# Kernel optimization log

Hardware: AMD Instinct MI355X
Metric: run time of the kernel (lower is better)

Reference implementation:

```python
import jax, jax.numpy as jnp
import numpy as np


def setup_inputs() -> dict:
    key = jax.random.key(0)
    k1, k2 = jax.random.split(key)
    bs, dim = 8192, 768
    nl_vec = jax.random.normal(k1, (bs, dim), dtype=jnp.float32)
    code_vec = jax.random.normal(k2, (bs, dim), dtype=jnp.float32)
    return {"nl_vec": nl_vec, "code_vec": code_vec}


def reference(nl_vec, code_vec):
    # scores[i, j] = <nl_vec[i], code_vec[j]>  (GEMM form of the broadcast mult-sum)
    scores = jnp.einsum("id,jd->ij", nl_vec, code_vec)  # [bs, bs]
    bs = scores.shape[0]
    # CrossEntropyLoss with labels = arange(bs): mean over rows of (logsumexp - diag)
    lse = jax.nn.logsumexp(scores, axis=-1)             # [bs]
    diag = jnp.einsum("id,id->i", nl_vec, code_vec)     # scores[i, i]
    loss = jnp.mean(lse - diag)
    return (loss, code_vec, nl_vec)
```

## Files before the change

### kernel.cpp

```cpp
#include <hip/hip_runtime.h>

#define BS     8192
#define DIM    768
#define NPART  16
#define BM     128
#define BN     128
#define BK     64
#define PCOLS  (BS / NPART)
#define NJT    (PCOLS / BN)
#define NKT    (DIM / BK)
#define L1B    128
#define L1R    (BS / L1B)

typedef __bf16 bfrag_t __attribute__((ext_vector_type(8)));
typedef float  facc_t  __attribute__((ext_vector_type(4)));

typedef const __attribute__((address_space(1))) void gv_t;
typedef __attribute__((address_space(3))) void lv_t;

__device__ __forceinline__ void gll16(const void* g, void* l) {
  __builtin_amdgcn_global_load_lds((gv_t*)g, (lv_t*)l, 16, 0, 0);
}

__device__ __forceinline__ unsigned short f2bf(float f) {
  union { float f; unsigned u; } v; v.f = f;
  unsigned u = v.u;
  return (unsigned short)((u + 0x7FFFu + ((u >> 16) & 1u)) >> 16);
}

__global__ void prep_kernel(const float* __restrict__ nl, const float* __restrict__ cd,
                            float* __restrict__ cd_copy, float* __restrict__ nl_copy,
                            unsigned short* __restrict__ nlb, unsigned short* __restrict__ cdb,
                            float* __restrict__ dg) {
  const int lane = threadIdx.x & 63;
  const int wave = threadIdx.x >> 6;
  const int row  = blockIdx.x * 4 + wave;
  const size_t rbase = (size_t)row * DIM;
  const float4* ar = reinterpret_cast<const float4*>(nl + rbase);
  const float4* br = reinterpret_cast<const float4*>(cd + rbase);
  float4* wa = reinterpret_cast<float4*>(nl_copy + rbase);
  float4* wb = reinterpret_cast<float4*>(cd_copy + rbase);
  ushort4* ba = reinterpret_cast<ushort4*>(nlb + rbase);
  ushort4* bb = reinterpret_cast<ushort4*>(cdb + rbase);

  float s = 0.f;
#pragma unroll
  for (int i = 0; i < 3; ++i) {
    int idx = lane + 64 * i;
    float4 x = ar[idx];
    float4 y = br[idx];
    wa[idx] = x;
    wb[idx] = y;
    ushort4 xb, yb;
    xb.x = f2bf(x.x); xb.y = f2bf(x.y); xb.z = f2bf(x.z); xb.w = f2bf(x.w);
    yb.x = f2bf(y.x); yb.y = f2bf(y.y); yb.z = f2bf(y.z); yb.w = f2bf(y.w);
    ba[idx] = xb;
    bb[idx] = yb;
    s += x.x * y.x + x.y * y.y + x.z * y.z + x.w * y.w;
  }
#pragma unroll
  for (int off = 32; off; off >>= 1) s += __shfl_xor(s, off, 64);
  if (lane == 0) dg[row] = s;
}

__global__ __launch_bounds__(256, 4) void gemm_lse_kernel(
    const unsigned short* __restrict__ Abf,
    const unsigned short* __restrict__ Bbf,
    float* __restrict__ pm, float* __restrict__ pl) {
  __shared__ __align__(16) unsigned short As[BM * BK];
  __shared__ __align__(16) unsigned short Bs[BN * BK];

  const int tid  = threadIdx.x;
  const int lane = tid & 63;
  const int wave = tid >> 6;
  const int wm   = wave >> 1;
  const int wn   = wave & 1;
  const int l15  = lane & 15;
  const int l4   = lane >> 4;
  const int sw   = l15 & 7;
  const int cp   = blockIdx.x;
  const int rb   = blockIdx.y;

  int srow[4], sc8g[4];
#pragma unroll
  for (int t = 0; t < 4; ++t) {
    int u   = wave * 256 + t * 64 + lane;
    srow[t] = u >> 3;
    sc8g[t] = (u & 7) ^ (srow[t] & 7);
  }

  float mrun[4][4], lrun[4][4];
#pragma unroll
  for (int i = 0; i < 4; ++i)
#pragma unroll
    for (int r = 0; r < 4; ++r) { mrun[i][r] = -1e30f; lrun[i][r] = 0.f; }

  for (int jt = 0; jt < NJT; ++jt) {
    facc_t acc[4][4];
#pragma unroll
    for (int mt = 0; mt < 4; ++mt)
#pragma unroll
      for (int nt = 0; nt < 4; ++nt) acc[mt][nt] = (facc_t){0.f, 0.f, 0.f, 0.f};

    for (int kt = 0; kt < NKT; ++kt) {
      __syncthreads();
#pragma unroll
      for (int t = 0; t < 4; ++t) {
        size_t ldso = (size_t)(wave * 256 + t * 64) * 8;
        gll16(Abf + (size_t)(rb * BM + srow[t]) * DIM + kt * BK + sc8g[t] * 8, As + ldso);
        gll16(Bbf + (size_t)(cp * PCOLS + jt * BN + srow[t]) * DIM + kt * BK + sc8g[t] * 8, Bs + ldso);
      }
      __syncthreads();

#pragma unroll
      for (int ks = 0; ks < 2; ++ks) {
        const int k8 = ks * 4 + l4;
        bfrag_t af[4], bfv[4];
#pragma unroll
        for (int mt = 0; mt < 4; ++mt) {
          int row = wm * 64 + mt * 16 + l15;
          af[mt] = *reinterpret_cast<const bfrag_t*>(&As[row * BK + (k8 ^ sw) * 8]);
        }
#pragma unroll
        for (int nt = 0; nt < 4; ++nt) {
          int row = wn * 64 + nt * 16 + l15;
          bfv[nt] = *reinterpret_cast<const bfrag_t*>(&Bs[row * BK + (k8 ^ sw) * 8]);
        }
#pragma unroll
        for (int mt = 0; mt < 4; ++mt)
#pragma unroll
          for (int nt = 0; nt < 4; ++nt)
            acc[mt][nt] = __builtin_amdgcn_mfma_f32_16x16x32_bf16(af[mt], bfv[nt], acc[mt][nt], 0, 0, 0);
      }
    }

#pragma unroll
    for (int mt = 0; mt < 4; ++mt)
#pragma unroll
      for (int r = 0; r < 4; ++r) {
        float v0 = acc[mt][0][r], v1 = acc[mt][1][r], v2 = acc[mt][2][r], v3 = acc[mt][3][r];
        float tm = fmaxf(fmaxf(v0, v1), fmaxf(v2, v3));
        float mn = fmaxf(mrun[mt][r], tm);
        float sc = __expf(mrun[mt][r] - mn);
        lrun[mt][r] = lrun[mt][r] * sc +
                      __expf(v0 - mn) + __expf(v1 - mn) + __expf(v2 - mn) + __expf(v3 - mn);
        mrun[mt][r] = mn;
      }
  }

#pragma unroll
  for (int mask = 1; mask < 16; mask <<= 1)
#pragma unroll
    for (int mt = 0; mt < 4; ++mt)
#pragma unroll
      for (int r = 0; r < 4; ++r) {
        float om = __shfl_xor(mrun[mt][r], mask, 64);
        float ol = __shfl_xor(lrun[mt][r], mask, 64);
        float mn = fmaxf(mrun[mt][r], om);
        lrun[mt][r] = lrun[mt][r] * __expf(mrun[mt][r] - mn) + ol * __expf(om - mn);
        mrun[mt][r] = mn;
      }

  float* cm = reinterpret_cast<float*>(As);
  float* cl = reinterpret_cast<float*>(Bs);
  __syncthreads();
  if (l15 == 0) {
#pragma unroll
    for (int mt = 0; mt < 4; ++mt)
#pragma unroll
      for (int r = 0; r < 4; ++r) {
        int rl = wm * 64 + mt * 16 + l4 * 4 + r;
        cm[wn * BM + rl] = mrun[mt][r];
        cl[wn * BM + rl] = lrun[mt][r];
      }
  }
  __syncthreads();
  if (tid < BM) {
    float m0 = cm[tid], l0 = cl[tid];
    float m1 = cm[BM + tid], l1 = cl[BM + tid];
    float mn = fmaxf(m0, m1);
    float ll = l0 * __expf(m0 - mn) + l1 * __expf(m1 - mn);
    size_t g = (size_t)(rb * BM + tid) * NPART + cp;
    pm[g] = mn;
    pl[g] = ll;
  }
}

__global__ void loss_stage1_kernel(const float* __restrict__ pm, const float* __restrict__ pl,
                                   const float* __restrict__ dg, float* __restrict__ partial) {
  __shared__ float red[64];
  const int tid = threadIdx.x;
  const int r   = blockIdx.x * L1R + tid;

  const float4* pmr = reinterpret_cast<const float4*>(pm + (size_t)r * NPART);
  const float4* plr = reinterpret_cast<const float4*>(pl + (size_t)r * NPART);

  float m = -1e30f, l = 0.f;
#pragma unroll
  for (int q = 0; q < NPART / 4; ++q) {
    float4 mv = pmr[q];
    float4 lv = plr[q];
#pragma unroll
    for (int k = 0; k < 4; ++k) {
      float m2 = (&mv.x)[k], l2 = (&lv.x)[k];
      float mn = fmaxf(m, m2);
      l = l * __expf(m - mn) + l2 * __expf(m2 - mn);
      m = mn;
    }
  }
  float local = m + __logf(l) - dg[r];

#pragma unroll
  for (int off = 32; off; off >>= 1) local += __shfl_xor(local, off, 64);
  if (tid == 0) partial[blockIdx.x] = local;
  (void)red;
}

__global__ void loss_stage2_kernel(const float* __restrict__ partial, float* __restrict__ out) {
  const int tid = threadIdx.x;
  float v = partial[tid];
#pragma unroll
  for (int off = 32; off; off >>= 1) v += __shfl_xor(v, off, 64);
  __shared__ float red[2];
  if ((tid & 63) == 0) red[tid >> 6] = v;
  __syncthreads();
  if (tid == 0) out[0] = (red[0] + red[1]) / (float)BS;
}

extern "C" void kernel_launch(void* const* d_in, const int* in_sizes, int n_in,
                              void* d_out, int out_size, void* d_ws, size_t ws_size,
                              hipStream_t stream) {
  const float* nl = (const float*)d_in[0];
  const float* cd = (const float*)d_in[1];
  float* out = (float*)d_out;

  const size_t NEL = (size_t)BS * DIM;

  unsigned short* nlb = (unsigned short*)d_ws;
  unsigned short* cdb = nlb + NEL;
  float* pm = (float*)(cdb + NEL);
  float* pl = pm + (size_t)BS * NPART;
  float* dg = pl + (size_t)BS * NPART;
  float* partial = dg + BS;

  prep_kernel<<<BS / 4, 256, 0, stream>>>(nl, cd, out + 1, out + 1 + NEL, nlb, cdb, dg);
  gemm_lse_kernel<<<dim3(NPART, BS / BM), 256, 0, stream>>>(nlb, cdb, pm, pl);
  loss_stage1_kernel<<<L1B, 64, 0, stream>>>(pm, pl, dg, partial);
  loss_stage2_kernel<<<1, 128, 0, stream>>>(partial, out);
}
```

Baseline: 226.5 us.

## Move output passthrough copies into GEMM prologue and merge loss reduction kernels

The fp32 copies of code_vec and nl_vec into the output buffer move out of the prep kernel and into the start of the GEMM kernel. There they run as aligned float4 stores that shift the data by one element, so the copy traffic can overlap with compute-bound GEMM blocks. The two loss reduction kernels become one kernel that ends in an atomicAdd, and out[0] is zeroed in the GEMM prologue. This removes a launch and shortens the prep kernel, but it adds memory traffic to the GEMM kernel. Correctness relies on the GEMM kernel zeroing out[0] before the loss kernel runs.

```diff
diff --git a/kernel.cpp b/kernel.cpp
--- a/kernel.cpp
+++ b/kernel.cpp
@@ -9,8 +9,9 @@
 #define PCOLS  (BS / NPART)
 #define NJT    (PCOLS / BN)
 #define NKT    (DIM / BK)
-#define L1B    128
-#define L1R    (BS / L1B)
+#define NEL    ((size_t)BS * DIM)
+#define NEL4   (NEL / 4)
+#define CTILE  (2 * NEL4 - 1)
 
 typedef __bf16 bfrag_t __attribute__((ext_vector_type(8)));
 typedef float  facc_t  __attribute__((ext_vector_type(4)));
@@ -29,7 +30,6 @@
 }
 
 __global__ void prep_kernel(const float* __restrict__ nl, const float* __restrict__ cd,
-                            float* __restrict__ cd_copy, float* __restrict__ nl_copy,
                             unsigned short* __restrict__ nlb, unsigned short* __restrict__ cdb,
                             float* __restrict__ dg) {
   const int lane = threadIdx.x & 63;
@@ -38,8 +38,6 @@
   const size_t rbase = (size_t)row * DIM;
   const float4* ar = reinterpret_cast<const float4*>(nl + rbase);
   const float4* br = reinterpret_cast<const float4*>(cd + rbase);
-  float4* wa = reinterpret_cast<float4*>(nl_copy + rbase);
-  float4* wb = reinterpret_cast<float4*>(cd_copy + rbase);
   ushort4* ba = reinterpret_cast<ushort4*>(nlb + rbase);
   ushort4* bb = reinterpret_cast<ushort4*>(cdb + rbase);
 
@@ -49,8 +47,6 @@
     int idx = lane + 64 * i;
     float4 x = ar[idx];
     float4 y = br[idx];
-    wa[idx] = x;
-    wb[idx] = y;
     ushort4 xb, yb;
     xb.x = f2bf(x.x); xb.y = f2bf(x.y); xb.z = f2bf(x.z); xb.w = f2bf(x.w);
     yb.x = f2bf(y.x); yb.y = f2bf(y.y); yb.z = f2bf(y.z); yb.w = f2bf(y.w);
@@ -63,9 +59,15 @@
   if (lane == 0) dg[row] = s;
 }
 
+__device__ __forceinline__ float4 cc4(const float4* cd4, const float4* nl4, size_t i) {
+  return (i < NEL4) ? cd4[i] : nl4[i - NEL4];
+}
+
 __global__ __launch_bounds__(256, 4) void gemm_lse_kernel(
     const unsigned short* __restrict__ Abf,
     const unsigned short* __restrict__ Bbf,
+    const float* __restrict__ cdf, const float* __restrict__ nlf,
+    float* __restrict__ outp,
     float* __restrict__ pm, float* __restrict__ pl) {
   __shared__ __align__(16) unsigned short As[BM * BK];
   __shared__ __align__(16) unsigned short Bs[BN * BK];
@@ -81,6 +83,25 @@
   const int cp   = blockIdx.x;
   const int rb   = blockIdx.y;
 
+  {
+    const float4* cd4 = reinterpret_cast<const float4*>(cdf);
+    const float4* nl4 = reinterpret_cast<const float4*>(nlf);
+    const size_t gtid = ((size_t)blockIdx.y * gridDim.x + blockIdx.x) * blockDim.x + tid;
+    const size_t nthr = (size_t)gridDim.x * gridDim.y * blockDim.x;
+    for (size_t m = 1 + gtid; m <= CTILE; m += nthr) {
+      float4 A = cc4(cd4, nl4, m - 1);
+      float4 B = cc4(cd4, nl4, m);
+      float4 d;
+      d.x = A.w; d.y = B.x; d.z = B.y; d.w = B.z;
+      *reinterpret_cast<float4*>(outp + 4 * m) = d;
+    }
+    if (gtid == 0) {
+      outp[0] = 0.f;
+      outp[1] = cdf[0]; outp[2] = cdf[1]; outp[3] = cdf[2];
+      outp[2 * NEL] = nlf[NEL - 1];
+    }
+  }
+
   int srow[4], sc8g[4];
 #pragma unroll
   for (int t = 0; t < 4; ++t) {
@@ -186,11 +207,11 @@
   }
 }
 
-__global__ void loss_stage1_kernel(const float* __restrict__ pm, const float* __restrict__ pl,
-                                   const float* __restrict__ dg, float* __restrict__ partial) {
-  __shared__ float red[64];
+__global__ void loss_kernel(const float* __restrict__ pm, const float* __restrict__ pl,
+                            const float* __restrict__ dg, float* __restrict__ out) {
+  __shared__ float red[4];
   const int tid = threadIdx.x;
-  const int r   = blockIdx.x * L1R + tid;
+  const int r   = blockIdx.x * 256 + tid;
 
   const float4* pmr = reinterpret_cast<const float4*>(pm + (size_t)r * NPART);
   const float4* plr = reinterpret_cast<const float4*>(pl + (size_t)r * NPART);
@@ -212,19 +233,12 @@
 
 #pragma unroll
   for (int off = 32; off; off >>= 1) local += __shfl_xor(local, off, 64);
-  if (tid == 0) partial[blockIdx.x] = local;
-  (void)red;
-}
-
-__global__ void loss_stage2_kernel(const float* __restrict__ partial, float* __restrict__ out) {
-  const int tid = threadIdx.x;
-  float v = partial[tid];
-#pragma unroll
-  for (int off = 32; off; off >>= 1) v += __shfl_xor(v, off, 64);
-  __shared__ float red[2];
-  if ((tid & 63) == 0) red[tid >> 6] = v;
+  if ((tid & 63) == 0) red[tid >> 6] = local;
   __syncthreads();
-  if (tid == 0) out[0] = (red[0] + red[1]) / (float)BS;
+  if (tid == 0) {
+    float s = red[0] + red[1] + red[2] + red[3];
+    atomicAdd(out, s / (float)BS);
+  }
 }
 
 extern "C" void kernel_launch(void* const* d_in, const int* in_sizes, int n_in,
@@ -234,17 +248,13 @@
   const float* cd = (const float*)d_in[1];
   float* out = (float*)d_out;
 
-  const size_t NEL = (size_t)BS * DIM;
-
   unsigned short* nlb = (unsigned short*)d_ws;
   unsigned short* cdb = nlb + NEL;
   float* pm = (float*)(cdb + NEL);
   float* pl = pm + (size_t)BS * NPART;
   float* dg = pl + (size_t)BS * NPART;
-  float* partial = dg + BS;
-
-  prep_kernel<<<BS / 4, 256, 0, stream>>>(nl, cd, out + 1, out + 1 + NEL, nlb, cdb, dg);
-  gemm_lse_kernel<<<dim3(NPART, BS / BM), 256, 0, stream>>>(nlb, cdb, pm, pl);
-  loss_stage1_kernel<<<L1B, 64, 0, stream>>>(pm, pl, dg, partial);
-  loss_stage2_kernel<<<1, 128, 0, stream>>>(partial, out);
-}
+
+  prep_kernel<<<BS / 4, 256, 0, stream>>>(nl, cd, nlb, cdb, dg);
+  gemm_lse_kernel<<<dim3(NPART, BS / BM), 256, 0, stream>>>(nlb, cdb, cd, nl, out, pm, pl);
+  loss_kernel<<<BS / 256, 256, 0, stream>>>(pm, pl, dg, out);
+}
```

Result: no change. 226.7 us (+0.1%).
